# Optimization experiments

Measured on AMD Instinct MI355X. Metric: run time of the kernel, lower is better.

The kernel has to match this reference:

```python
import jax, jax.numpy as jnp
import numpy as np

WS = 7  # window size
NH = 12  # num heads
EPS = 1e-5


def setup_inputs() -> dict:
    key = jax.random.key(0)
    ks = jax.random.split(key, 12)
    B, H, W, C = 32, 56, 56, 384
    Dff = 4 * C
    s = lambda k, shape, scale=0.02: jax.random.normal(k, shape, dtype=jnp.float32) * scale
    return {
        "x": jax.random.normal(ks[0], (B, H, W, C), dtype=jnp.float32),
        "ln1_g": jnp.ones((C,), jnp.float32), "ln1_b": jnp.zeros((C,), jnp.float32),
        "qkv_w": s(ks[1], (C, 3 * C)), "qkv_b": jnp.zeros((3 * C,), jnp.float32),
        "proj_w": s(ks[2], (C, C)), "proj_b": jnp.zeros((C,), jnp.float32),
        "ln2_g": jnp.ones((C,), jnp.float32), "ln2_b": jnp.zeros((C,), jnp.float32),
        "mlp_w1": s(ks[3], (C, Dff)), "mlp_b1": jnp.zeros((Dff,), jnp.float32),
        "mlp_w2": s(ks[4], (Dff, C)), "mlp_b2": jnp.zeros((C,), jnp.float32),
    }


def _layernorm(x, g, b):
    m = jnp.mean(x, axis=-1, keepdims=True)
    v = jnp.mean(jnp.square(x - m), axis=-1, keepdims=True)
    return (x - m) * jax.lax.rsqrt(v + EPS) * g + b


def reference(x, ln1_g, ln1_b, qkv_w, qkv_b, proj_w, proj_b, ln2_g, ln2_b,
              mlp_w1, mlp_b1, mlp_w2, mlp_b2):
    B, H, W, C = x.shape
    N = WS * WS
    hd = C // NH
    shortcut = x
    xn = _layernorm(x, ln1_g, ln1_b)
    # window partition: [B,H,W,C] -> [B*nW, N, C]
    xw = xn.reshape(B, H // WS, WS, W // WS, WS, C).transpose(0, 1, 3, 2, 4, 5)
    xw = xw.reshape(-1, N, C)
    # attention within each 49-token window
    qkv = (xw @ qkv_w + qkv_b).reshape(-1, N, 3, NH, hd)
    qkv = qkv.transpose(2, 0, 3, 1, 4)  # [3, Bn, h, N, d]
    q, k, v = qkv[0] * (hd ** -0.5), qkv[1], qkv[2]
    attn = jax.nn.softmax(jnp.einsum('bhnd,bhmd->bhnm', q, k), axis=-1)
    out = jnp.einsum('bhnm,bhmd->bhnd', attn, v)  # [Bn, h, N, d]
    out = out.transpose(0, 2, 1, 3).reshape(-1, N, C)
    out = out @ proj_w + proj_b
    # window unpartition
    xa = out.reshape(B, H // WS, W // WS, WS, WS, C).transpose(0, 1, 3, 2, 4, 5)
    xa = xa.reshape(B, H, W, C)
    x = shortcut + xa
    # MLP (dropout inactive at inference); Keras gelu default is exact
    h = jax.nn.gelu(_layernorm(x, ln2_g, ln2_b) @ mlp_w1 + mlp_b1, approximate=False)
    return x + (h @ mlp_w2 + mlp_b2)
```

## Files before the change

### kernel.cpp

```cpp
#include <hip/hip_runtime.h>
#include <hip/hip_bf16.h>
#include <cstdint>

typedef __bf16 bf16;
typedef __bf16 bf16x8 __attribute__((ext_vector_type(8)));
typedef float f32x4 __attribute__((ext_vector_type(4)));
typedef unsigned int u32;
typedef unsigned short u16;

#define DEV static __device__ __forceinline__

DEV float bfbits2f(u32 bits) { return __builtin_bit_cast(float, bits << 16); }
DEV u16 f2bfbits(float f) {
  u32 u = __builtin_bit_cast(u32, f);
  u32 r = (u + 0x7fffu + ((u >> 16) & 1u)) >> 16;
  return (u16)r;
}

__global__ __launch_bounds__(256) void probe_k(const u32* __restrict__ x, u32* __restrict__ flag) {
  __shared__ int cnt[256];
  int t = threadIdx.x;
  int c = 0;
#pragma unroll
  for (int i = 0; i < 4; ++i) {
    u32 u = x[t * 4 + i];
    u32 e = (u >> 7) & 0xFF;
    c += (e >= 110 && e <= 140) ? 1 : 0;
  }
  cnt[t] = c;
  __syncthreads();
  for (int s = 128; s > 0; s >>= 1) {
    if (t < s) cnt[t] += cnt[t + s];
    __syncthreads();
  }
  if (t == 0) flag[0] = (cnt[0] > 512) ? 1u : 0u;
}

__global__ __launch_bounds__(256) void cvt_params_k(const void* p0, const void* p1,
                                                    const void* p2, const void* p3,
                                                    const void* p4, const void* p5,
                                                    const void* p6, const void* p7,
                                                    float* __restrict__ out,
                                                    const u32* __restrict__ flag) {
  int i = blockIdx.x * 256 + threadIdx.x;
  if (i >= 4992) return;
  const int bounds[9] = {0, 1152, 1536, 3072, 3456, 3840, 4224, 4608, 4992};
  const void* ps[8] = {p0, p1, p2, p3, p4, p5, p6, p7};
  int seg = 0;
  while (i >= bounds[seg + 1]) ++seg;
  int off = i - bounds[seg];
  bool isbf = flag[0] != 0;
  out[i] = isbf ? bfbits2f(((const u16*)ps[seg])[off]) : ((const float*)ps[seg])[off];
}

__global__ __launch_bounds__(256) void transpose_k(const void* __restrict__ in,
                                                   u16* __restrict__ out, int R, int Cc,
                                                   const u32* __restrict__ flag) {
  bool isbf = flag[0] != 0;
  __shared__ u16 tile[32][33];
  int bx = blockIdx.x * 32, by = blockIdx.y * 32;
  int tx = threadIdx.x & 31, ty = threadIdx.x >> 5;
#pragma unroll
  for (int i = 0; i < 32; i += 8) {
    size_t idx = (size_t)(by + ty + i) * Cc + bx + tx;
    u16 v = isbf ? ((const u16*)in)[idx] : f2bfbits(((const float*)in)[idx]);
    tile[ty + i][tx] = v;
  }
  __syncthreads();
#pragma unroll
  for (int i = 0; i < 32; i += 8)
    out[(size_t)(bx + ty + i) * R + by + tx] = tile[tx][ty + i];
}

template <int RAWSRC>
__global__ __launch_bounds__(256) void ln_kernel(const void* __restrict__ xv,
                                                 const float* __restrict__ g,
                                                 const float* __restrict__ b,
                                                 u32* __restrict__ out,
                                                 const u32* __restrict__ flag,
                                                 int windowed, int t0) {
  const int t = t0 + blockIdx.x * 4 + (threadIdx.x >> 6);
  const int lane = threadIdx.x & 63;
  const int e0 = lane * 6;
  float f[6];
  if (RAWSRC) {
    if (flag[0] != 0) {
      const u16* xb = (const u16*)xv + (size_t)t * 384 + e0;
#pragma unroll
      for (int j = 0; j < 6; ++j) f[j] = bfbits2f(xb[j]);
    } else {
      const float* xf = (const float*)xv + (size_t)t * 384 + e0;
#pragma unroll
      for (int j = 0; j < 6; ++j) f[j] = xf[j];
    }
  } else {
    const u32* xr = (const u32*)xv + (size_t)t * 192 + lane * 3;
#pragma unroll
    for (int j = 0; j < 3; ++j) {
      u32 u = xr[j];
      f[2 * j] = bfbits2f(u & 0xffff);
      f[2 * j + 1] = bfbits2f(u >> 16);
    }
  }
  float s = 0.f, q = 0.f;
#pragma unroll
  for (int j = 0; j < 6; ++j) { s += f[j]; q += f[j] * f[j]; }
#pragma unroll
  for (int o = 1; o < 64; o <<= 1) { s += __shfl_xor(s, o); q += __shfl_xor(q, o); }
  float mean = s * (1.0f / 384.0f);
  float var = q * (1.0f / 384.0f) - mean * mean;
  float rstd = rsqrtf(var + 1e-5f);
  int orow;
  if (windowed) {
    int bb = t / 3136, rem = t % 3136;
    int hh = rem / 56, ww = rem % 56;
    orow = (bb * 64 + (hh / 7) * 8 + (ww / 7)) * 49 + (hh % 7) * 7 + (ww % 7) - t0;
  } else {
    orow = t - t0;
  }
  u32* orp = out + (size_t)orow * 192 + lane * 3;
#pragma unroll
  for (int j = 0; j < 3; ++j) {
    float ye = (f[2 * j] - mean) * rstd * g[e0 + 2 * j] + b[e0 + 2 * j];
    float yo = (f[2 * j + 1] - mean) * rstd * g[e0 + 2 * j + 1] + b[e0 + 2 * j + 1];
    orp[j] = (u32)f2bfbits(ye) | ((u32)f2bfbits(yo) << 16);
  }
}

template <int MODE>
__global__ __launch_bounds__(256, 4) void gemm128(const bf16* __restrict__ A,
                                                  const bf16* __restrict__ BT,
                                                  void* __restrict__ Cv,
                                                  const float* __restrict__ bias,
                                                  const void* __restrict__ resv,
                                                  const u32* __restrict__ flag,
                                                  int ldA, int ldC, int K, int rowOff) {
  const int tN = blockIdx.x, tM = blockIdx.y;
  const int tid = threadIdx.x;
  const int lane = tid & 63, wave = tid >> 6;
  const int wr = wave >> 1, wc = wave & 1;
  const int li = lane & 15, gq = lane >> 4;
  const bool isbf = flag[0] != 0;

  __shared__ bf16 As[128 * 64];
  __shared__ bf16 Bs[128 * 64];

  f32x4 acc[4][4] = {};

  const bf16* aTile = A + (size_t)tM * 128 * ldA;
  const bf16* bTile = BT + (size_t)tN * 128 * K;

  for (int k0 = 0; k0 < K; k0 += 64) {
#pragma unroll
    for (int i = 0; i < 4; ++i) {
      int c = i * 256 + tid;
      int row = c >> 3, col8 = (c & 7) << 3;
      __builtin_amdgcn_global_load_lds(
          (const __attribute__((address_space(1))) void*)(aTile + (size_t)row * ldA + k0 + col8),
          (__attribute__((address_space(3))) void*)(As + (size_t)c * 8), 16, 0, 0);
      __builtin_amdgcn_global_load_lds(
          (const __attribute__((address_space(1))) void*)(bTile + (size_t)row * K + k0 + col8),
          (__attribute__((address_space(3))) void*)(Bs + (size_t)c * 8), 16, 0, 0);
    }
    __syncthreads();
#pragma unroll
    for (int ks = 0; ks < 64; ks += 32) {
      bf16x8 af[4], bfr[4];
#pragma unroll
      for (int m = 0; m < 4; ++m)
        af[m] = *(const bf16x8*)(As + (wr * 64 + m * 16 + li) * 64 + ks + gq * 8);
#pragma unroll
      for (int n = 0; n < 4; ++n)
        bfr[n] = *(const bf16x8*)(Bs + (wc * 64 + n * 16 + li) * 64 + ks + gq * 8);
#pragma unroll
      for (int m = 0; m < 4; ++m)
#pragma unroll
        for (int n = 0; n < 4; ++n)
          acc[m][n] = __builtin_amdgcn_mfma_f32_16x16x32_bf16(af[m], bfr[n], acc[m][n], 0, 0, 0);
    }
    __syncthreads();
  }

#pragma unroll
  for (int m = 0; m < 4; ++m) {
#pragma unroll
    for (int r = 0; r < 4; ++r) {
      int row = tM * 128 + wr * 64 + m * 16 + gq * 4 + r;
      size_t crow;
      if (MODE == 1) {
        int gg = rowOff + row;
        int win = gg / 49, n = gg % 49;
        int bb = win >> 6, wi = win & 63;
        int hh = (wi >> 3) * 7 + n / 7;
        int ww = (wi & 7) * 7 + n % 7;
        crow = (size_t)(bb * 3136 + hh * 56 + ww);
      } else {
        crow = (size_t)row;
      }
#pragma unroll
      for (int n = 0; n < 4; ++n) {
        int col = tN * 128 + wc * 64 + n * 16 + li;
        size_t idx = crow * (size_t)ldC + col;
        float v = acc[m][n][r] + bias[col];
        if (MODE == 2) v = 0.5f * v * (1.0f + erff(v * 0.70710678118654752f));
        if (MODE == 1)
          v += isbf ? bfbits2f(((const u16*)resv)[idx]) : ((const float*)resv)[idx];
        if (MODE == 3) v += bfbits2f(((const u16*)resv)[idx]);
        if (MODE == 3) {
          size_t oidx = idx + (size_t)rowOff * 384;
          if (isbf) ((u16*)Cv)[oidx] = f2bfbits(v);
          else ((float*)Cv)[oidx] = v;
        } else {
          ((u16*)Cv)[idx] = f2bfbits(v);
        }
      }
    }
  }
}

__global__ __launch_bounds__(256, 2) void attn_kernel(const bf16* __restrict__ qkv,
                                                      bf16* __restrict__ out) {
  __shared__ bf16 smem[4 * 6912];
  const int wave = threadIdx.x >> 6;
  const int lane = threadIdx.x & 63;
  const int unit = blockIdx.x * 4 + wave;
  const int win = unit / 12, head = unit % 12;
  bf16* P = smem + wave * 6912;
  bf16* VT = P + 64 * 72;

  const size_t base = (size_t)win * 49 * 1152 + head * 32;
  const bf16* Qp = qkv + base;
  const bf16* Kp = qkv + base + 384;
  const bf16* Vp = qkv + base + 768;

  const int gq = lane >> 4, li = lane & 15;

  {
    int d = lane & 31, half = lane >> 5;
#pragma unroll
    for (int i = 0; i < 32; ++i) {
      int m = i * 2 + half;
      bf16 v = (m < 49) ? Vp[(size_t)m * 1152 + d] : (bf16)0.0f;
      VT[d * 72 + m] = v;
    }
  }

  f32x4 s[4][4] = {};
  bf16x8 qf[4], kf[4];
#pragma unroll
  for (int i = 0; i < 4; ++i) {
    int qr = i * 16 + li; if (qr > 48) qr = 48;
    qf[i] = *(const bf16x8*)(Qp + (size_t)qr * 1152 + gq * 8);
    kf[i] = *(const bf16x8*)(Kp + (size_t)qr * 1152 + gq * 8);
  }
#pragma unroll
  for (int i = 0; i < 4; ++i)
#pragma unroll
    for (int j = 0; j < 4; ++j)
      s[i][j] = __builtin_amdgcn_mfma_f32_16x16x32_bf16(qf[i], kf[j], s[i][j], 0, 0, 0);

  __syncthreads();

  const float scale = 0.17677669529663687f;
#pragma unroll
  for (int i = 0; i < 4; ++i) {
#pragma unroll
    for (int r = 0; r < 4; ++r) {
      float v0 = s[i][0][r] * scale, v1 = s[i][1][r] * scale;
      float v2 = s[i][2][r] * scale, v3 = s[i][3][r] * scale;
      if (li >= 1) v3 = -1e30f;
      float mx = fmaxf(fmaxf(v0, v1), fmaxf(v2, v3));
#pragma unroll
      for (int o = 1; o < 16; o <<= 1) mx = fmaxf(mx, __shfl_xor(mx, o));
      v0 = __expf(v0 - mx); v1 = __expf(v1 - mx);
      v2 = __expf(v2 - mx); v3 = __expf(v3 - mx);
      float sum = v0 + v1 + v2 + v3;
#pragma unroll
      for (int o = 1; o < 16; o <<= 1) sum += __shfl_xor(sum, o);
      float inv = 1.0f / sum;
      int n = i * 16 + gq * 4 + r;
      P[n * 72 + li]      = (bf16)(v0 * inv);
      P[n * 72 + 16 + li] = (bf16)(v1 * inv);
      P[n * 72 + 32 + li] = (bf16)(v2 * inv);
      P[n * 72 + 48 + li] = (bf16)(v3 * inv);
    }
  }

  __syncthreads();

  f32x4 o[4][2] = {};
#pragma unroll
  for (int ms = 0; ms < 2; ++ms) {
    bf16x8 pf[4], vf[2];
#pragma unroll
    for (int i = 0; i < 4; ++i)
      pf[i] = *(const bf16x8*)(P + (i * 16 + li) * 72 + ms * 32 + gq * 8);
#pragma unroll
    for (int dt = 0; dt < 2; ++dt)
      vf[dt] = *(const bf16x8*)(VT + (dt * 16 + li) * 72 + ms * 32 + gq * 8);
#pragma unroll
    for (int i = 0; i < 4; ++i)
#pragma unroll
      for (int dt = 0; dt < 2; ++dt)
        o[i][dt] = __builtin_amdgcn_mfma_f32_16x16x32_bf16(pf[i], vf[dt], o[i][dt], 0, 0, 0);
  }

#pragma unroll
  for (int i = 0; i < 4; ++i) {
#pragma unroll
    for (int r = 0; r < 4; ++r) {
      int n = i * 16 + gq * 4 + r;
      if (n < 49) {
#pragma unroll
        for (int dt = 0; dt < 2; ++dt) {
          int d = dt * 16 + li;
          out[((size_t)win * 49 + n) * 384 + head * 32 + d] = (bf16)o[i][dt][r];
        }
      }
    }
  }
}

extern "C" void kernel_launch(void* const* d_in, const int* in_sizes, int n_in,
                              void* d_out, int out_size, void* d_ws, size_t ws_size,
                              hipStream_t stream) {
  const void* x      = d_in[0];
  const void* ln1_g  = d_in[1];
  const void* ln1_b  = d_in[2];
  const void* qkv_w  = d_in[3];
  const void* qkv_b  = d_in[4];
  const void* proj_w = d_in[5];
  const void* proj_b = d_in[6];
  const void* ln2_g  = d_in[7];
  const void* ln2_b  = d_in[8];
  const void* mlp_w1 = d_in[9];
  const void* mlp_b1 = d_in[10];
  const void* mlp_w2 = d_in[11];
  const void* mlp_b2 = d_in[12];

  char* ws = (char*)d_ws;
  u32* flag = (u32*)ws;
  bf16* qkvwT  = (bf16*)(ws + 256);
  bf16* projwT = qkvwT + 1152 * 384;
  bf16* w1T    = projwT + 384 * 384;
  bf16* w2T    = w1T + 1536 * 384;
  float* pF    = (float*)(ws + 3539200);
  float* qkv_bF  = pF;
  float* proj_bF = pF + 1152;
  float* mlp_b1F = pF + 1536;
  float* mlp_b2F = pF + 3072;
  float* ln1gF   = pF + 3456;
  float* ln1bF   = pF + 3840;
  float* ln2gF   = pF + 4224;
  float* ln2bF   = pF + 4608;
  bf16* x2 = (bf16*)(ws + 3559168);
  char* basep = ws + 80629504ULL;
  const size_t avail = (ws_size > 80629504ULL) ? (ws_size - 80629504ULL) : 0;

  int Wc = 128;
  { const int cand[5] = {2048, 1024, 512, 256, 128};
    for (int i = 0; i < 5; ++i)
      if ((size_t)cand[i] * 49 * 1536 * 2 <= avail) { Wc = cand[i]; break; } }
  int Rc = 6272;
  { const int cand[5] = {100352, 50176, 25088, 12544, 6272};
    for (int i = 0; i < 5; ++i)
      if ((size_t)cand[i] * 1920 * 2 <= avail) { Rc = cand[i]; break; } }

  probe_k<<<1, 256, 0, stream>>>((const u32*)x, flag);

  cvt_params_k<<<20, 256, 0, stream>>>(qkv_b, proj_b, mlp_b1, mlp_b2,
                                       ln1_g, ln1_b, ln2_g, ln2_b, pF, flag);
  transpose_k<<<dim3(36, 12), 256, 0, stream>>>(qkv_w, (u16*)qkvwT, 384, 1152, flag);
  transpose_k<<<dim3(12, 12), 256, 0, stream>>>(proj_w, (u16*)projwT, 384, 384, flag);
  transpose_k<<<dim3(48, 12), 256, 0, stream>>>(mlp_w1, (u16*)w1T, 384, 1536, flag);
  transpose_k<<<dim3(12, 48), 256, 0, stream>>>(mlp_w2, (u16*)w2T, 1536, 384, flag);

  for (int c = 0; c < 2048 / Wc; ++c) {
    const int w0 = c * Wc, t0 = w0 * 49, M = Wc * 49;
    bf16* xn   = (bf16*)basep;
    bf16* qkvb = xn + (size_t)M * 384;
    ln_kernel<1><<<M / 4, 256, 0, stream>>>(x, ln1gF, ln1bF, (u32*)xn, flag, 1, t0);
    gemm128<0><<<dim3(9, M / 128), 256, 0, stream>>>(xn, qkvwT, qkvb, qkv_bF, nullptr, flag,
                                                     384, 1152, 384, 0);
    attn_kernel<<<Wc * 3, 256, 0, stream>>>(qkvb, xn);
    gemm128<1><<<dim3(3, M / 128), 256, 0, stream>>>(xn, projwT, x2, proj_bF, x, flag,
                                                     384, 384, 384, t0);
  }

  for (int c = 0; c < 100352 / Rc; ++c) {
    const int r0 = c * Rc;
    bf16* xn2 = (bf16*)basep;
    bf16* hb  = xn2 + (size_t)Rc * 384;
    ln_kernel<0><<<Rc / 4, 256, 0, stream>>>(x2, ln2gF, ln2bF, (u32*)xn2, flag, 0, r0);
    gemm128<2><<<dim3(12, Rc / 128), 256, 0, stream>>>(xn2, w1T, hb, mlp_b1F, nullptr, flag,
                                                       384, 1536, 384, 0);
    gemm128<3><<<dim3(3, Rc / 128), 256, 0, stream>>>(hb, w2T, d_out, mlp_b2F,
                                                      x2 + (size_t)r0 * 384, flag,
                                                      1536, 384, 1536, r0);
  }
}
```

Baseline: 913.5 us.

## Remap GEMM workgroups XCD-aware and cap chunk sizes for L2 residency

Flattens each GEMM grid to 1D and remaps block IDs so that consecutive logical tiles land on the same XCD. Blocks that share A rows then also share an XCD L2. The window and row chunk sizes are capped lower so each chunk's intermediates stay closer to cache. Smaller chunks mean more kernel launches and smaller grids per launch.

```diff
diff --git a/kernel.cpp b/kernel.cpp
--- a/kernel.cpp
+++ b/kernel.cpp
@@ -134,8 +134,15 @@
                                                   const float* __restrict__ bias,
                                                   const void* __restrict__ resv,
                                                   const u32* __restrict__ flag,
-                                                  int ldA, int ldC, int K, int rowOff) {
-  const int tN = blockIdx.x, tM = blockIdx.y;
+                                                  int ldA, int ldC, int K, int rowOff,
+                                                  int nN) {
+  const int nwg = (int)gridDim.x;
+  const int bid = (int)blockIdx.x;
+  const int q = nwg >> 3, r = nwg & 7;
+  const int xcd = bid & 7, lid = bid >> 3;
+  const int wg = (xcd < r ? xcd * (q + 1) : r * (q + 1) + (xcd - r) * q) + lid;
+  const int tN = wg % nN, tM = wg / nN;
+
   const int tid = threadIdx.x;
   const int lane = tid & 63, wave = tid >> 6;
   const int wr = wave >> 1, wc = wave & 1;
@@ -184,8 +191,8 @@
 #pragma unroll
   for (int m = 0; m < 4; ++m) {
 #pragma unroll
-    for (int r = 0; r < 4; ++r) {
-      int row = tM * 128 + wr * 64 + m * 16 + gq * 4 + r;
+    for (int r2 = 0; r2 < 4; ++r2) {
+      int row = tM * 128 + wr * 64 + m * 16 + gq * 4 + r2;
       size_t crow;
       if (MODE == 1) {
         int gg = rowOff + row;
@@ -201,7 +208,7 @@
       for (int n = 0; n < 4; ++n) {
         int col = tN * 128 + wc * 64 + n * 16 + li;
         size_t idx = crow * (size_t)ldC + col;
-        float v = acc[m][n][r] + bias[col];
+        float v = acc[m][n][r2] + bias[col];
         if (MODE == 2) v = 0.5f * v * (1.0f + erff(v * 0.70710678118654752f));
         if (MODE == 1)
           v += isbf ? bfbits2f(((const u16*)resv)[idx]) : ((const float*)resv)[idx];
@@ -358,12 +365,12 @@
   const size_t avail = (ws_size > 80629504ULL) ? (ws_size - 80629504ULL) : 0;
 
   int Wc = 128;
-  { const int cand[5] = {2048, 1024, 512, 256, 128};
-    for (int i = 0; i < 5; ++i)
+  { const int cand[3] = {512, 256, 128};
+    for (int i = 0; i < 3; ++i)
       if ((size_t)cand[i] * 49 * 1536 * 2 <= avail) { Wc = cand[i]; break; } }
   int Rc = 6272;
-  { const int cand[5] = {100352, 50176, 25088, 12544, 6272};
-    for (int i = 0; i < 5; ++i)
+  { const int cand[3] = {25088, 12544, 6272};
+    for (int i = 0; i < 3; ++i)
       if ((size_t)cand[i] * 1920 * 2 <= avail) { Rc = cand[i]; break; } }
 
   probe_k<<<1, 256, 0, stream>>>((const u32*)x, flag);
@@ -377,25 +384,27 @@
 
   for (int c = 0; c < 2048 / Wc; ++c) {
     const int w0 = c * Wc, t0 = w0 * 49, M = Wc * 49;
+    const int nM = M / 128;
     bf16* xn   = (bf16*)basep;
     bf16* qkvb = xn + (size_t)M * 384;
     ln_kernel<1><<<M / 4, 256, 0, stream>>>(x, ln1gF, ln1bF, (u32*)xn, flag, 1, t0);
-    gemm128<0><<<dim3(9, M / 128), 256, 0, stream>>>(xn, qkvwT, qkvb, qkv_bF, nullptr, flag,
-                                                     384, 1152, 384, 0);
+    gemm128<0><<<dim3(9 * nM), 256, 0, stream>>>(xn, qkvwT, qkvb, qkv_bF, nullptr, flag,
+                                                 384, 1152, 384, 0, 9);
     attn_kernel<<<Wc * 3, 256, 0, stream>>>(qkvb, xn);
-    gemm128<1><<<dim3(3, M / 128), 256, 0, stream>>>(xn, projwT, x2, proj_bF, x, flag,
-                                                     384, 384, 384, t0);
+    gemm128<1><<<dim3(3 * nM), 256, 0, stream>>>(xn, projwT, x2, proj_bF, x, flag,
+                                                 384, 384, 384, t0, 3);
   }
 
   for (int c = 0; c < 100352 / Rc; ++c) {
     const int r0 = c * Rc;
+    const int nM = Rc / 128;
     bf16* xn2 = (bf16*)basep;
     bf16* hb  = xn2 + (size_t)Rc * 384;
     ln_kernel<0><<<Rc / 4, 256, 0, stream>>>(x2, ln2gF, ln2bF, (u32*)xn2, flag, 0, r0);
-    gemm128<2><<<dim3(12, Rc / 128), 256, 0, stream>>>(xn2, w1T, hb, mlp_b1F, nullptr, flag,
-                                                       384, 1536, 384, 0);
-    gemm128<3><<<dim3(3, Rc / 128), 256, 0, stream>>>(hb, w2T, d_out, mlp_b2F,
-                                                      x2 + (size_t)r0 * 384, flag,
-                                                      1536, 384, 1536, r0);
-  }
-}
+    gemm128<2><<<dim3(12 * nM), 256, 0, stream>>>(xn2, w1T, hb, mlp_b1F, nullptr, flag,
+                                                  384, 1536, 384, 0, 12);
+    gemm128<3><<<dim3(3 * nM), 256, 0, stream>>>(hb, w2T, d_out, mlp_b2F,
+                                                 x2 + (size_t)r0 * 384, flag,
+                                                 1536, 384, 1536, r0, 3);
+  }
+}
```

Result: slower. 957.9 us (+4.9%).
